# Kernel optimization log

Hardware: AMD Instinct MI355X
Metric: run time of the kernel (lower is better)

Reference implementation:

```python
import jax, jax.numpy as jnp
import numpy as np
from jax.scipy.linalg import solve_triangular

B, K, N = 64, 24, 934  # batch, SMPL joints (key_size), sparse mesh points (A_size)
LAMBDA_FACTOR = 1.0


def _rodrigues(rvec):
    # rvec: [..., 3] axis-angle -> [..., 3, 3] rotation matrix (SMPL rodrigues)
    theta = jnp.maximum(jnp.linalg.norm(rvec, axis=-1, keepdims=True), 1e-8)
    a = rvec / theta
    c = jnp.cos(theta)[..., None]
    s = jnp.sin(theta)[..., None]
    ax, ay, az = a[..., 0], a[..., 1], a[..., 2]
    zero = jnp.zeros_like(ax)
    skew = jnp.stack([
        jnp.stack([zero, -az, ay], -1),
        jnp.stack([az, zero, -ax], -1),
        jnp.stack([-ay, ax, zero], -1)], -2)
    aaT = a[..., :, None] * a[..., None, :]
    eye = jnp.eye(3, dtype=rvec.dtype)
    return c * eye + s * skew + (1.0 - c) * aaT


def setup_inputs() -> dict:
    key = jax.random.key(0)
    ks = jax.random.split(key, 8)
    return {
        "uv_curr": jax.random.uniform(ks[0], (B, N, 2), jnp.float32),
        "xm_": jax.random.normal(ks[1], (B, K, N, 3), jnp.float32),
        "b_s_": jax.random.normal(ks[2], (B, K, N, 3, 10), jnp.float32) * 0.1,
        "blend_curr": jax.random.uniform(ks[3], (N, K), jnp.float32),
        "W": jax.random.uniform(ks[4], (B, N), jnp.float32) * 0.95 + 0.05,
        "m00": jnp.ones((B,), jnp.float32),
        "m11": jnp.ones((B,), jnp.float32),
        "m02": jax.random.uniform(ks[5], (B,), jnp.float32),
        "m12": jax.random.uniform(ks[6], (B,), jnp.float32),
        "pred_beta": jax.random.normal(ks[7], (B, 10), jnp.float32),
        "valid_R_list_stack": jnp.broadcast_to(jnp.eye(4, dtype=jnp.float32), (B, K, 4, 4)),
    }


def reference(uv_curr, xm_, b_s_, blend_curr, W, m00, m11, m02, m12, pred_beta, valid_R_list_stack):
    Bn, Kn, Nn = xm_.shape[0], xm_.shape[1], xm_.shape[2]
    lam = jnp.exp(jnp.log(jnp.float32(1.0 / 3.0)) * jnp.float32(LAMBDA_FACTOR))  # k0*exp(log(k0/3)*lf)

    bT = blend_curr.T[None]                      # [1,K,N]
    f0 = m00[:, None, None]                       # [B,1,1]
    f1 = m11[:, None, None]
    dxu = (m02[:, None] - uv_curr[..., 0])[:, None]  # [B,1,N]
    dyv = (m12[:, None] - uv_curr[..., 1])[:, None]

    x1 = dxu * xm_[..., 1]
    x2 = f0 * xm_[..., 2] - dxu * xm_[..., 0]
    x3 = -f0 * xm_[..., 1]
    x8 = jnp.broadcast_to(bT * f0, (Bn, Kn, Nn))
    x9 = jnp.zeros((Bn, Kn, Nn), xm_.dtype)
    x10 = jnp.broadcast_to(bT * dxu, (Bn, Kn, Nn))
    y1 = -f1 * xm_[..., 2] + dyv * xm_[..., 1]
    y2 = -dyv * xm_[..., 0]
    y3 = f1 * xm_[..., 0]
    y8 = x9
    y9 = jnp.broadcast_to(bT * f1, (Bn, Kn, Nn))
    y10 = jnp.broadcast_to(bT * dyv, (Bn, Kn, Nn))

    # shape-beta blocks: [B,K,N,10]
    x4a = f0[..., None] * b_s_[:, :, :, 0] + dxu[..., None] * b_s_[:, :, :, 2]
    y4a = f1[..., None] * b_s_[:, :, :, 1] + dyv[..., None] * b_s_[:, :, :, 2]

    b1 = -f0 * xm_[..., 0] - dxu * xm_[..., 2]
    b2 = -f1 * xm_[..., 1] - dyv * xm_[..., 2]

    # [B,K,N,6] -> [B,N,K*6]
    A1 = jnp.stack([x1, x2, x3, x8, x9, x10], -1).transpose(0, 2, 1, 3).reshape(Bn, Nn, Kn * 6)
    A2 = jnp.stack([y1, y2, y3, y8, y9, y10], -1).transpose(0, 2, 1, 3).reshape(Bn, Nn, Kn * 6)
    Wn = W[..., None]
    A_top = jnp.concatenate([Wn * A1, Wn * A2], 1)            # [B,2N,6K]
    A_sh = jnp.concatenate([Wn * x4a.sum(1), Wn * y4a.sum(1)], 1)  # [B,2N,10]
    b_top = jnp.concatenate([W * b1.sum(1), W * b2.sum(1)], 1)     # [B,2N]

    rows = 2 * Nn + 10 + 3 * Kn + 3
    cols = 6 * Kn + 10
    A = jnp.zeros((Bn, rows, cols), jnp.float32)
    A = A.at[:, :2 * Nn, :6 * Kn].set(A_top)
    A = A.at[:, :2 * Nn, 6 * Kn:].set(A_sh)
    ridx = jnp.arange(10)
    A = A.at[:, rows - 10 + ridx, cols - 10 + ridx].set(lam)  # beta regularizer
    Bv = jnp.zeros((Bn, rows), jnp.float32)
    Bv = Bv.at[:, :2 * Nn].set(b_top)
    Bv = Bv.at[:, rows - 10:].set(lam * pred_beta)

    # least squares via reduced QR (same as torch train path / lstsq solution)
    q, r = jnp.linalg.qr(A)                       # q:[B,rows,cols], r:[B,cols,cols]
    rhs = jnp.einsum('bmn,bm->bn', q, Bv)
    sol = solve_triangular(r, rhs[..., None], lower=False)[..., 0]  # [B,6K+10]

    rt6 = sol[:, :6 * Kn].reshape(Bn, Kn, 6)
    r_pred = _rodrigues(rt6[..., :3])             # [B,K,3,3]
    t_pred = rt6[..., 3:]                         # [B,K,3]
    bottom = jnp.broadcast_to(jnp.array([0.0, 0.0, 0.0, 1.0], jnp.float32), (Bn, Kn, 1, 4))
    rt_pred = jnp.concatenate([
        jnp.concatenate([r_pred, jnp.zeros((Bn, Kn, 3, 1), jnp.float32)], -1),
        bottom], -2)                               # [B,K,4,4]
    r_curr = rt_pred @ valid_R_list_stack
    beta = sol[:, -10:]
    return (r_curr, t_pred, beta, r_pred)
```

## Files before the change

kernel.cpp:

```cpp
#include <hip/hip_runtime.h>
#include <hip/hip_bf16.h>

#define Bn 64
#define Kn 24
#define Nn 934
#define NBLK 4
#define GCH 234
#define NPTS 16
#define RNDS 15
#define GPK 12090
#define PB 11
#define NPAN 14
#define ST 512
#define STR 168
#define GT 512
#define MAXT 9

#define G_BYTES ((size_t)Bn * GPK * 8)

typedef __attribute__((ext_vector_type(4))) double f64x4;

__device__ __forceinline__ int rb(int i) { return (i * (i + 1)) >> 1; }

__global__ __launch_bounds__(1024) void k_pre(
    const float* __restrict__ uv, const float* __restrict__ xm,
    const float* __restrict__ bs, const float* __restrict__ Wp,
    const float* __restrict__ m00, const float* __restrict__ m11,
    const float* __restrict__ m02, const float* __restrict__ m12,
    float* __restrict__ pre)
{
    __shared__ float smL[32][30];
    __shared__ float xsL[32][3];
    const int tid = threadIdx.x;
    const int b = blockIdx.y;
    const int n0 = blockIdx.x * 32;
    const float f0 = m00[b], f1 = m11[b], cx = m02[b], cy = m12[b];

    if (tid < 960) {
        const int ni = tid / 30, c = tid - ni * 30;
        const int nc = min(n0 + ni, Nn - 1);
        float acc = 0.0f;
        const float* bp = bs + ((size_t)(b * Kn) * Nn + nc) * 30 + c;
        #pragma unroll
        for (int k = 0; k < Kn; ++k) acc += bp[(size_t)k * Nn * 30];
        smL[ni][c] = acc;
    } else {
        const int v = tid - 960;
        #pragma unroll
        for (int rep = 0; rep < 2; ++rep) {
            const int w = v + rep * 64;
            if (w < 96) {
                const int ni = w / 3, c = w - ni * 3;
                const int nc = min(n0 + ni, Nn - 1);
                float acc = 0.0f;
                const float* xp = xm + ((size_t)(b * Kn) * Nn + nc) * 3 + c;
                #pragma unroll
                for (int k = 0; k < Kn; ++k) acc += xp[(size_t)k * Nn * 3];
                xsL[ni][c] = acc;
            }
        }
    }
    __syncthreads();

    if (tid < 704) {
        const int ni = tid / 22, e = tid - ni * 22;
        const int n = n0 + ni;
        if (n < Nn) {
            const float u = uv[((size_t)b * Nn + n) * 2 + 0];
            const float v = uv[((size_t)b * Nn + n) * 2 + 1];
            const float w = Wp[(size_t)b * Nn + n];
            const float dxu = cx - u, dyv = cy - v;
            float val;
            if (e < 10)       val = w * (f0 * smL[ni][e] + dxu * smL[ni][20 + e]);
            else if (e < 20)  val = w * (f1 * smL[ni][e] + dyv * smL[ni][e + 10]);
            else if (e == 20) val = w * (-f0 * xsL[ni][0] - dxu * xsL[ni][2]);
            else              val = w * (-f1 * xsL[ni][1] - dyv * xsL[ni][2]);
            pre[((size_t)b * Nn + n) * 22 + e] = val;
        }
    }
}

__global__ __launch_bounds__(GT, 1) void k_gram(
    const float* __restrict__ uv, const float* __restrict__ xm,
    const float* __restrict__ blend, const float* __restrict__ Wp,
    const float* __restrict__ m00, const float* __restrict__ m11,
    const float* __restrict__ m02, const float* __restrict__ m12,
    const float* __restrict__ pre, double* __restrict__ Gpk)
{
    __shared__ float rowsF[2][2 * NPTS][STR];
    const int tid = threadIdx.x;
    const int b = blockIdx.y;
    const int n0 = blockIdx.x * GCH;
    const int nEnd = min(n0 + GCH, Nn);
    const float f0 = m00[b], f1 = m11[b], cx = m02[b], cy = m12[b];

    const int pt = (tid >> 4) & 15, s = tid & 15;
    const int wave = tid >> 6, lane = tid & 63;

    const f64x4 zz = {0.0, 0.0, 0.0, 0.0};
    const f64x4 pr = __builtin_amdgcn_mfma_f64_16x16x4f64((double)lane, 1.0, zz, 0, 0, 0);
    const f64x4 pc = __builtin_amdgcn_mfma_f64_16x16x4f64(1.0, (double)lane, zz, 0, 0, 0);
    const int v0 = (int)pr[0];
    const bool ac0 = (v0 >= 96) && (v0 <= 156) && (((v0 - 96) & 3) == 0);
    const int arow = ac0 ? (lane & 15) : (lane >> 2);
    const int ak   = ac0 ? (lane >> 4) : (lane & 3);
    const int w0 = (int)pc[0];
    const bool bc0 = (w0 >= 96) && (w0 <= 156) && (((w0 - 96) & 3) == 0);
    const int bcol = bc0 ? (lane & 15) : (lane >> 2);
    const int bk   = bc0 ? (lane >> 4) : (lane & 3);
    int orow[4], ocol[4];
    #pragma unroll
    for (int r2 = 0; r2 < 4; ++r2) {
        const int vr = (int)pr[r2];
        orow[r2] = ac0 ? ((vr - 96) >> 2) : ((vr - 6) >> 4);
        const int wr = (int)pc[r2];
        ocol[r2] = bc0 ? ((wr - 96) >> 2) : ((wr - 6) >> 4);
    }

    const int t0 = (wave < 4) ? wave * 5 : 20 + (wave - 4) * 9;
    const int cnt = (wave < 4) ? 5 : 9;
    int Ia[MAXT], Ja[MAXT];
    {
        int Iv = 0, Jv = t0;
        while (Jv > Iv) { Jv -= (Iv + 1); ++Iv; }
        #pragma unroll
        for (int t = 0; t < MAXT; ++t) {
            Ia[t] = Iv; Ja[t] = Jv;
            ++Jv;
            if (Jv > Iv) { Jv = 0; ++Iv; }
        }
    }

    f64x4 acc[MAXT];
    #pragma unroll
    for (int t = 0; t < MAXT; ++t) acc[t] = (f64x4){0.0, 0.0, 0.0, 0.0};

    float pf[11];
    const bool isBd = tid < 256;

    auto PF = [&](int rnd) {
        if (!isBd) return;
        const int nc = min(n0 + rnd * NPTS + pt, Nn - 1);
        if (s < 12) {
            const int k0 = 2 * s;
            const float* xa = xm + ((size_t)(b * Kn + k0) * Nn + nc) * 3;
            const float* xb = xm + ((size_t)(b * Kn + k0 + 1) * Nn + nc) * 3;
            pf[0] = xa[0]; pf[1] = xa[1]; pf[2] = xa[2];
            pf[3] = xb[0]; pf[4] = xb[1]; pf[5] = xb[2];
            pf[6] = blend[nc * Kn + k0];
            pf[7] = blend[nc * Kn + k0 + 1];
            pf[8] = uv[((size_t)b * Nn + nc) * 2 + 0];
            pf[9] = uv[((size_t)b * Nn + nc) * 2 + 1];
            pf[10] = Wp[(size_t)b * Nn + nc];
        } else if (s < 15) {
            const int e0 = (s - 12) * 8;
            const float* pp = pre + ((size_t)b * Nn + nc) * 22;
            #pragma unroll
            for (int j = 0; j < 8; ++j) pf[j] = (e0 + j < 22) ? pp[e0 + j] : 0.0f;
        }
    };
    auto WR = [&](int rnd, int bufi) {
        if (!isBd) return;
        const int n = n0 + rnd * NPTS + pt;
        float* rx = &rowsF[bufi][2 * pt][0];
        float* ry = &rowsF[bufi][2 * pt + 1][0];
        if (s < 12) {
            #pragma unroll
            for (int jj = 0; jj < 2; ++jj) {
                float vx[6], vy[6];
                if (n < nEnd) {
                    const float x0 = pf[jj * 3 + 0], x1 = pf[jj * 3 + 1], x2 = pf[jj * 3 + 2];
                    const float dxu = cx - pf[8], dyv = cy - pf[9], w = pf[10];
                    const float wbl = w * pf[6 + jj];
                    vx[0] = w * dxu * x1; vx[1] = w * (f0 * x2 - dxu * x0); vx[2] = -w * f0 * x1;
                    vx[3] = wbl * f0;     vx[4] = 0.0f;                     vx[5] = wbl * dxu;
                    vy[0] = w * (dyv * x1 - f1 * x2); vy[1] = -w * dyv * x0; vy[2] = w * f1 * x0;
                    vy[3] = 0.0f;         vy[4] = wbl * f1;                 vy[5] = wbl * dyv;
                } else {
                    #pragma unroll
                    for (int e = 0; e < 6; ++e) { vx[e] = 0.0f; vy[e] = 0.0f; }
                }
                const int cb = 6 * (2 * s + jj);
                #pragma unroll
                for (int e = 0; e < 6; ++e) {
                    rx[cb + e] = vx[e];
                    ry[cb + e] = vy[e];
                }
            }
        } else if (s < 15) {
            const int e0 = (s - 12) * 8;
            #pragma unroll
            for (int j = 0; j < 8; ++j) {
                const int e = e0 + j;
                if (e < 22) {
                    const float val = (n < nEnd) ? pf[j] : 0.0f;
                    if (e < 10)       rx[144 + e] = val;
                    else if (e < 20)  ry[144 + (e - 10)] = val;
                    else if (e == 20) rx[154] = val;
                    else              ry[154] = val;
                }
            }
        }
    };

    for (int idx = tid; idx < 320; idx += GT) {
        const int bufi = idx / 160, rem = idx % 160;
        rowsF[bufi][rem / 5][155 + rem % 5] = 0.0f;
    }

    PF(0);
    WR(0, 0);
    PF(1);
    __syncthreads();

    for (int r = 0; r < RNDS; ++r) {
        const int cur = r & 1;
        if (r < RNDS - 1) {
            WR(r + 1, cur ^ 1);
            if (r + 2 < RNDS) PF(r + 2);
        }
        #pragma unroll
        for (int ksl = 0; ksl < 8; ++ksl) {
            const float* rowA = &rowsF[cur][4 * ksl + ak][0];
            const float* rowB = &rowsF[cur][4 * ksl + bk][0];
            #pragma unroll
            for (int t = 0; t < MAXT; ++t) {
                if (t < cnt && t0 + t < 55) {
                    const double av = (double)rowA[16 * Ia[t] + arow];
                    const double bv = (double)rowB[16 * Ja[t] + bcol];
                    acc[t] = __builtin_amdgcn_mfma_f64_16x16x4f64(av, bv, acc[t], 0, 0, 0);
                }
            }
        }
        __syncthreads();
    }

    double* Gb = Gpk + (size_t)b * GPK;
    #pragma unroll
    for (int t = 0; t < MAXT; ++t) {
        if (t < cnt && t0 + t < 55) {
            #pragma unroll
            for (int rr = 0; rr < 4; ++rr) {
                const int gi = 16 * Ia[t] + orow[rr];
                const int gj = 16 * Ja[t] + ocol[rr];
                if (gi < 155 && gj < 155 && gj <= gi)
                    unsafeAtomicAdd(&Gb[rb(gi) + gj], acc[t][rr]);
            }
        }
    }
}

__global__ __launch_bounds__(ST) void k_solve(
    const float* __restrict__ pbeta, const float* __restrict__ vR,
    const double* __restrict__ Gpk, float* __restrict__ out)
{
    __shared__ double tri[11935];
    __shared__ double fd[NPAN][66];
    __shared__ double Pp[143][PB];
    __shared__ double Qq[143][PB];
    __shared__ double cv[160];
    __shared__ double xv[160];
    __shared__ double dinv[160];
    const int tid = threadIdx.x;
    const int b = blockIdx.x;
    const double lam2 = 1.0 / 9.0;
    const double* Gb = Gpk + (size_t)b * GPK;

    for (int idx = tid; idx < 11935; idx += ST) tri[idx] = Gb[idx];
    for (int r = tid; r < 154; r += ST) {
        double c0v = Gb[11935 + r];
        if (r >= 144) c0v += lam2 * (double)pbeta[b * 10 + (r - 144)];
        cv[r] = c0v;
    }
    __syncthreads();
    if (tid < 10) { const int d = 144 + tid; tri[rb(d) + d] += lam2; }
    __syncthreads();

    for (int p = 0; p < NPAN; ++p) {
        const int c0 = p * PB, r0 = c0 + PB, m = 154 - r0;

        double dblk[66], dl[PB];
        #pragma unroll
        for (int r = 0; r < PB; ++r) {
            const int baser = rb(c0 + r) + c0;
            #pragma unroll
            for (int c = 0; c <= r; ++c) dblk[r * (r + 1) / 2 + c] = tri[baser + c];
        }
        #pragma unroll
        for (int j = 0; j < PB; ++j) {
            const double invd = 1.0 / dblk[j * (j + 1) / 2 + j];
            dl[j] = invd;
            #pragma unroll
            for (int r = j + 1; r < PB; ++r) {
                const double mr = dblk[r * (r + 1) / 2 + j] * invd;
                #pragma unroll
                for (int c = j + 1; c <= r; ++c)
                    dblk[r * (r + 1) / 2 + c] -= mr * dblk[c * (c + 1) / 2 + j];
            }
        }
        if (tid == 0) {
            #pragma unroll
            for (int e = 0; e < 66; ++e) fd[p][e] = dblk[e];
            #pragma unroll
            for (int j = 0; j < PB; ++j) dinv[c0 + j] = dl[j];
        }

        if (m > 0) {
            for (int i = r0 + tid; i < 154; i += ST) {
                const int ip = i - r0;
                const int base = rb(i) + c0;
                double a[PB], bbv[PB];
                #pragma unroll
                for (int k = 0; k < PB; ++k) a[k] = tri[base + k];
                #pragma unroll
                for (int t = 0; t < PB; ++t) {
                    const double bt = a[t] * dl[t];
                    bbv[t] = bt;
                    #pragma unroll
                    for (int k = t + 1; k < PB; ++k)
                        a[k] -= bt * dblk[k * (k + 1) / 2 + t];
                }
                #pragma unroll
                for (int k = 0; k < PB; ++k) {
                    tri[base + k] = a[k]; Pp[ip][k] = bbv[k]; Qq[ip][k] = a[k];
                }
            }
            __syncthreads();
            const int tot = (m * (m + 1)) >> 1;
            for (int e = tid; e < tot; e += ST) {
                int row = (int)((sqrtf(8.0f * (float)e + 1.0f) - 1.0f) * 0.5f);
                while ((row + 1) * (row + 2) / 2 <= e) ++row;
                while (row * (row + 1) / 2 > e) --row;
                const int col = e - ((row * (row + 1)) >> 1);
                double sum = 0.0;
                #pragma unroll
                for (int k = 0; k < PB; ++k) sum += Pp[row][k] * Qq[col][k];
                tri[rb(r0 + row) + r0 + col] -= sum;
            }
        }
        __syncthreads();
    }

    for (int p = 0; p < NPAN; ++p) {
        const int c0 = p * PB, r0 = c0 + PB;
        double w[PB], dl[PB];
        #pragma unroll
        for (int r = 0; r < PB; ++r) { dl[r] = dinv[c0 + r]; w[r] = cv[c0 + r]; }
        #pragma unroll
        for (int t = 0; t < PB; ++t) {
            w[t] *= dl[t];
            #pragma unroll
            for (int k = t + 1; k < PB; ++k) w[k] -= fd[p][k * (k + 1) / 2 + t] * w[t];
        }
        if (tid == 0) {
            #pragma unroll
            for (int t = 0; t < PB; ++t) xv[c0 + t] = w[t];
        }
        for (int i = r0 + tid; i < 154; i += ST) {
            const int base = rb(i) + c0;
            double sum = 0.0;
            #pragma unroll
            for (int k = 0; k < PB; ++k) sum += tri[base + k] * w[k];
            cv[i] -= sum;
        }
        __syncthreads();
    }

    for (int p = NPAN - 1; p >= 0; --p) {
        const int c0 = p * PB;
        double x[PB], dl[PB];
        #pragma unroll
        for (int r = 0; r < PB; ++r) { dl[r] = dinv[c0 + r]; x[r] = xv[c0 + r]; }
        #pragma unroll
        for (int j = PB - 1; j >= 1; --j) {
            #pragma unroll
            for (int i2 = 0; i2 < j; ++i2)
                x[i2] -= dl[i2] * fd[p][j * (j + 1) / 2 + i2] * x[j];
        }
        if (tid == 0) {
            #pragma unroll
            for (int r = 0; r < PB; ++r) cv[c0 + r] = x[r];
        }
        for (int i = tid; i < c0; i += ST) {
            double sum = 0.0;
            #pragma unroll
            for (int jj = 0; jj < PB; ++jj) sum += tri[rb(c0 + jj) + i] * x[jj];
            xv[i] -= dinv[i] * sum;
        }
        __syncthreads();
    }

    if (tid < Kn) {
        const int k = tid;
        const double rxv = cv[6 * k + 0], ryv = cv[6 * k + 1], rzv = cv[6 * k + 2];
        const double t0 = cv[6 * k + 3], t1 = cv[6 * k + 4], t2 = cv[6 * k + 5];
        const double nrm = sqrt(rxv * rxv + ryv * ryv + rzv * rzv);
        const double th = fmax(nrm, 1e-8);
        const double ax = rxv / th, ay = ryv / th, az = rzv / th;
        const double c = cos(th), sn = sin(th), mc = 1.0 - c;
        double R[3][3];
        R[0][0] = c + mc * ax * ax;        R[0][1] = -sn * az + mc * ax * ay; R[0][2] =  sn * ay + mc * ax * az;
        R[1][0] =  sn * az + mc * ay * ax; R[1][1] = c + mc * ay * ay;        R[1][2] = -sn * ax + mc * ay * az;
        R[2][0] = -sn * ay + mc * az * ax; R[2][1] =  sn * ax + mc * az * ay; R[2][2] = c + mc * az * az;

        const float* VRp = vR + ((size_t)(b * Kn + k)) * 16;
        float* oc = out + ((size_t)(b * Kn + k)) * 16;
        #pragma unroll
        for (int r = 0; r < 3; ++r)
            #pragma unroll
            for (int cc = 0; cc < 4; ++cc) {
                const double val = R[r][0] * (double)VRp[0 * 4 + cc]
                                 + R[r][1] * (double)VRp[1 * 4 + cc]
                                 + R[r][2] * (double)VRp[2 * 4 + cc];
                oc[r * 4 + cc] = (float)val;
            }
        #pragma unroll
        for (int cc = 0; cc < 4; ++cc) oc[12 + cc] = VRp[12 + cc];

        float* ot = out + 24576 + ((size_t)(b * Kn + k)) * 3;
        ot[0] = (float)t0; ot[1] = (float)t1; ot[2] = (float)t2;

        float* orp = out + 29824 + ((size_t)(b * Kn + k)) * 9;
        #pragma unroll
        for (int r = 0; r < 3; ++r)
            #pragma unroll
            for (int cc = 0; cc < 3; ++cc)
                orp[r * 3 + cc] = (float)R[r][cc];
    }
    if (tid >= 32 && tid < 42) {
        out[29184 + b * 10 + (tid - 32)] = (float)cv[144 + (tid - 32)];
    }
}

extern "C" void kernel_launch(void* const* d_in, const int* in_sizes, int n_in,
                              void* d_out, int out_size, void* d_ws, size_t ws_size,
                              hipStream_t stream) {
    const float* uv    = (const float*)d_in[0];
    const float* xm    = (const float*)d_in[1];
    const float* bs    = (const float*)d_in[2];
    const float* blend = (const float*)d_in[3];
    const float* Wp    = (const float*)d_in[4];
    const float* m00   = (const float*)d_in[5];
    const float* m11   = (const float*)d_in[6];
    const float* m02   = (const float*)d_in[7];
    const float* m12   = (const float*)d_in[8];
    const float* pbeta = (const float*)d_in[9];
    const float* vRp   = (const float*)d_in[10];
    float* out = (float*)d_out;
    double* Gpk = (double*)d_ws;
    float* pre = (float*)((char*)d_ws + G_BYTES);

    hipMemsetAsync(d_ws, 0, G_BYTES, stream);

    dim3 gP((Nn + 31) / 32, Bn);
    k_pre<<<gP, 1024, 0, stream>>>(uv, xm, bs, Wp, m00, m11, m02, m12, pre);

    dim3 gG(NBLK, Bn);
    k_gram<<<gG, GT, 0, stream>>>(uv, xm, blend, Wp, m00, m11, m02, m12, pre, Gpk);

    k_solve<<<Bn, ST, 0, stream>>>(pbeta, vRp, Gpk, out);
}
```

Measured before the change: 259.3 us.

## Fold forward substitution into LDL factorization as augmented row; reorganize trailing update

```diff
diff --git a/kernel.cpp b/kernel.cpp
--- a/kernel.cpp
+++ b/kernel.cpp
@@ -254,10 +254,10 @@
     const float* __restrict__ pbeta, const float* __restrict__ vR,
     const double* __restrict__ Gpk, float* __restrict__ out)
 {
-    __shared__ double tri[11935];
+    __shared__ double tri[12090];
     __shared__ double fd[NPAN][66];
-    __shared__ double Pp[143][PB];
-    __shared__ double Qq[143][PB];
+    __shared__ double Pp[144][PB];
+    __shared__ double Qq[144][PB];
     __shared__ double cv[160];
     __shared__ double xv[160];
     __shared__ double dinv[160];
@@ -266,18 +266,18 @@
     const double lam2 = 1.0 / 9.0;
     const double* Gb = Gpk + (size_t)b * GPK;
 
-    for (int idx = tid; idx < 11935; idx += ST) tri[idx] = Gb[idx];
-    for (int r = tid; r < 154; r += ST) {
-        double c0v = Gb[11935 + r];
-        if (r >= 144) c0v += lam2 * (double)pbeta[b * 10 + (r - 144)];
-        cv[r] = c0v;
-    }
+    for (int idx = tid; idx < GPK; idx += ST) tri[idx] = Gb[idx];
     __syncthreads();
-    if (tid < 10) { const int d = 144 + tid; tri[rb(d) + d] += lam2; }
+    if (tid < 10) {
+        const int d = 144 + tid;
+        tri[rb(d) + d] += lam2;
+        tri[rb(154) + 144 + tid] += lam2 * (double)pbeta[b * 10 + tid];
+    }
     __syncthreads();
 
     for (int p = 0; p < NPAN; ++p) {
-        const int c0 = p * PB, r0 = c0 + PB, m = 154 - r0;
+        const int c0 = p * PB, r0 = c0 + PB;
+        const int m2 = 155 - r0;
 
         double dblk[66], dl[PB];
         #pragma unroll
@@ -305,66 +305,52 @@
             for (int j = 0; j < PB; ++j) dinv[c0 + j] = dl[j];
         }
 
-        if (m > 0) {
-            for (int i = r0 + tid; i < 154; i += ST) {
-                const int ip = i - r0;
-                const int base = rb(i) + c0;
-                double a[PB], bbv[PB];
+        for (int i = r0 + tid; i < 155; i += ST) {
+            const int ip = i - r0;
+            const int base = rb(i) + c0;
+            double a[PB], bbv[PB];
+            #pragma unroll
+            for (int k = 0; k < PB; ++k) a[k] = tri[base + k];
+            #pragma unroll
+            for (int t = 0; t < PB; ++t) {
+                const double bt = a[t] * dl[t];
+                bbv[t] = bt;
                 #pragma unroll
-                for (int k = 0; k < PB; ++k) a[k] = tri[base + k];
+                for (int k = t + 1; k < PB; ++k)
+                    a[k] -= bt * dblk[k * (k + 1) / 2 + t];
+            }
+            #pragma unroll
+            for (int k = 0; k < PB; ++k) {
+                tri[base + k] = a[k]; Pp[ip][k] = bbv[k]; Qq[ip][k] = a[k];
+            }
+        }
+        __syncthreads();
+
+        {
+            const int half = (m2 + 1) >> 1;
+            for (int q = tid; q < half; q += ST) {
                 #pragma unroll
-                for (int t = 0; t < PB; ++t) {
-                    const double bt = a[t] * dl[t];
-                    bbv[t] = bt;
+                for (int pass = 0; pass < 2; ++pass) {
+                    const int row = pass ? (m2 - 1 - q) : q;
+                    if (pass && row == q) break;
+                    double pp[PB];
                     #pragma unroll
-                    for (int k = t + 1; k < PB; ++k)
-                        a[k] -= bt * dblk[k * (k + 1) / 2 + t];
+                    for (int k = 0; k < PB; ++k) pp[k] = Pp[row][k];
+                    const int base = rb(r0 + row) + r0;
+                    for (int col = 0; col <= row; ++col) {
+                        double sum = 0.0;
+                        #pragma unroll
+                        for (int k = 0; k < PB; ++k) sum += pp[k] * Qq[col][k];
+                        tri[base + col] -= sum;
+                    }
                 }
-                #pragma unroll
-                for (int k = 0; k < PB; ++k) {
-                    tri[base + k] = a[k]; Pp[ip][k] = bbv[k]; Qq[ip][k] = a[k];
-                }
-            }
-            __syncthreads();
-            const int tot = (m * (m + 1)) >> 1;
-            for (int e = tid; e < tot; e += ST) {
-                int row = (int)((sqrtf(8.0f * (float)e + 1.0f) - 1.0f) * 0.5f);
-                while ((row + 1) * (row + 2) / 2 <= e) ++row;
-                while (row * (row + 1) / 2 > e) --row;
-                const int col = e - ((row * (row + 1)) >> 1);
-                double sum = 0.0;
-                #pragma unroll
-                for (int k = 0; k < PB; ++k) sum += Pp[row][k] * Qq[col][k];
-                tri[rb(r0 + row) + r0 + col] -= sum;
             }
         }
         __syncthreads();
     }
 
-    for (int p = 0; p < NPAN; ++p) {
-        const int c0 = p * PB, r0 = c0 + PB;
-        double w[PB], dl[PB];
-        #pragma unroll
-        for (int r = 0; r < PB; ++r) { dl[r] = dinv[c0 + r]; w[r] = cv[c0 + r]; }
-        #pragma unroll
-        for (int t = 0; t < PB; ++t) {
-            w[t] *= dl[t];
-            #pragma unroll
-            for (int k = t + 1; k < PB; ++k) w[k] -= fd[p][k * (k + 1) / 2 + t] * w[t];
-        }
-        if (tid == 0) {
-            #pragma unroll
-            for (int t = 0; t < PB; ++t) xv[c0 + t] = w[t];
-        }
-        for (int i = r0 + tid; i < 154; i += ST) {
-            const int base = rb(i) + c0;
-            double sum = 0.0;
-            #pragma unroll
-            for (int k = 0; k < PB; ++k) sum += tri[base + k] * w[k];
-            cv[i] -= sum;
-        }
-        __syncthreads();
-    }
+    for (int j = tid; j < 154; j += ST) xv[j] = tri[rb(154) + j] * dinv[j];
+    __syncthreads();
 
     for (int p = NPAN - 1; p >= 0; --p) {
         const int c0 = p * PB;
```

After: 328.2 us. +26.6%, slower.
